# Optimization experiments

Measured on AMD Instinct MI355X. Metric: run time of the kernel, lower is better.

## Reference

```python
import jax, jax.numpy as jnp
import numpy as np

N, T, V, C, O = 64, 512, 17, 3, 64
EPS = 1e-5  # torch BatchNorm eps


def _bn(x, gamma, beta):
    # training-mode BatchNorm2d over (N, H, W) per channel, biased variance
    m = jnp.mean(x, axis=(0, 2, 3), keepdims=True)
    v = jnp.var(x, axis=(0, 2, 3), keepdims=True)
    return gamma.reshape(1, -1, 1, 1) * (x - m) * jax.lax.rsqrt(v + EPS) + beta.reshape(1, -1, 1, 1)


def setup_inputs() -> dict:
    key = jax.random.key(0)
    ks = jax.random.split(key, 20)
    f32 = jnp.float32
    PA = (jnp.eye(V, dtype=f32) / (1.0 + 1e-5))  # row-normalized identity, as in reset_parameter
    return {
        "x": jax.random.normal(ks[0], (N, T, V, C), f32),
        "w1": jax.random.normal(ks[1], (C, C), f32) * 0.5,
        "b1": jax.random.normal(ks[2], (C,), f32) * 0.1,
        "w2": jax.random.normal(ks[3], (C, C), f32) * 0.5,
        "b2": jax.random.normal(ks[4], (C,), f32) * 0.1,
        "convT_w": jax.random.normal(ks[5], (C,), f32) * 0.5,      # Conv2d(3,1,1) weight squeezed
        "convT_b": jax.random.normal(ks[6], (), f32) * 0.1,
        "convT_gamma": jnp.ones((), f32),
        "convT_beta": jnp.zeros((), f32),
        "PA": PA,
        "alpha": jnp.ones((V, V), f32),
        "conv2d_w": jax.random.normal(ks[7], (O, C), f32) * (2.0 / (O * 1 * 1)) ** 0.5,  # conv_branch_init
        "conv2d_b": jnp.zeros((O,), f32),
        "bn_gamma": jnp.full((O,), 1e-6, f32),  # bn_init(self.bn, 1e-6)
        "bn_beta": jnp.zeros((O,), f32),
        "pool_w": jax.random.normal(ks[8], (O, C), f32) * (2.0 / C) ** 0.5,  # kaiming fan_out-ish
        "pool_b": jnp.zeros((O,), f32),
        "pool_gamma": jnp.ones((O,), f32),
        "pool_beta": jnp.zeros((O,), f32),
    }


def reference(x, w1, b1, w2, b2, convT_w, convT_b, convT_gamma, convT_beta,
              PA, alpha, conv2d_w, conv2d_b, bn_gamma, bn_beta,
              pool_w, pool_b, pool_gamma, pool_beta):
    # x: (N, T, V, C)
    x1 = x @ w1.T + b1                     # linear1, (N,T,V,C)
    x2 = x @ w2.T + b2                     # linear2
    # d[n,t,i,j,c] = x1[n,t,j,c] - x2[n,t,i,c]; the 1x1 conv over C is linear,
    # so contract with convT_w BEFORE broadcasting to avoid the (N,T,V,V,C) tensor.
    a1 = x1 @ convT_w                      # (N,T,V)
    a2 = x2 @ convT_w                      # (N,T,V)
    s = a1[:, :, None, :] - a2[:, :, :, None] + convT_b   # (N,T,V,V)
    # BatchNorm2d(1): single channel -> stats over the whole tensor; then ReLU
    m = jnp.mean(s)
    var = jnp.var(s)
    s = jax.nn.relu(convT_gamma * (s - m) * jax.lax.rsqrt(var + EPS) + convT_beta)
    # temporal abs-diff, sum over T, mean over batch -> learned adjacency offset (V,V)
    a3 = jnp.mean(jnp.sum(jnp.abs(s[:, 1:] - s[:, :-1]), axis=1), axis=0)
    # NOTE: the original does x.view(N, C, T, V) -- a raw memory reinterpretation,
    # NOT a permute. Replicate with reshape.
    xr = x.reshape(N, C, T, V)
    A = PA + alpha * a3                    # (V,V)
    y = (xr.reshape(N, C * T, V) @ A).reshape(N, C, T, V)
    z = jnp.einsum('nctv,oc->notv', y, conv2d_w) + conv2d_b[None, :, None, None]
    z = _bn(z, bn_gamma, bn_beta)
    p = jnp.einsum('nctv,oc->notv', xr, pool_w) + pool_b[None, :, None, None]
    p = _bn(p, pool_gamma, pool_beta)
    out = jax.nn.relu(z + p)               # (N,O,T,V)
    return out.reshape(N, T, V, O)         # raw reshape, matching torch .reshape
```

## Files before the change

kernel.cpp:

```cpp
#include <hip/hip_runtime.h>

constexpr int Nn = 64, Tt = 512, Vv = 17, Oo = 64;
constexpr int TV  = Tt * Vv;
constexpr int CTV = 3 * TV;
constexpr int NT  = Nn * Tt;
constexpr float EPSf = 1e-5f;
constexpr int GB1 = 512;
constexpr int RPB = 64;
constexpr int NU  = 289;
constexpr int GE  = 1792;
constexpr int TCH = 256;
constexpr int K2B = 128;
constexpr int BTV = 1088;

__device__ inline int div17(int v) { return (int)(((unsigned)v * 61681u) >> 20); }

__device__ inline double wred(double v) {
#pragma unroll
  for (int o = 32; o > 0; o >>= 1) v += __shfl_down(v, o, 64);
  return v;
}

__global__ void __launch_bounds__(256) k1(
    const float* __restrict__ x,
    const float* __restrict__ w1, const float* __restrict__ b1,
    const float* __restrict__ w2, const float* __restrict__ b2,
    const float* __restrict__ cw, const float* __restrict__ cb,
    double* __restrict__ spart, float* __restrict__ gpart)
{
  __shared__ float xsA[RPB * 51];
  __shared__ float xsB[3 * BTV];
  __shared__ double dred[4][5];
  const int tid = threadIdx.x, bid = blockIdx.x;
  const int n = bid >> 3, ch = bid & 7;

  {
    const float4* src = (const float4*)(x + (size_t)bid * 3264);
    float4* dst = (float4*)xsA;
    for (int i = tid; i < 816; i += 256) dst[i] = src[i];
  }
#pragma unroll
  for (int c = 0; c < 3; ++c) {
    const float4* src = (const float4*)(x + (size_t)n * CTV + (size_t)c * TV + ch * BTV);
    float4* dst = (float4*)(xsB + c * BTV);
    for (int i = tid; i < 272; i += 256) dst[i] = src[i];
  }
  __syncthreads();

  float u1[3], u2[3];
#pragma unroll
  for (int k = 0; k < 3; ++k) {
    float s1 = 0.f, s2 = 0.f;
#pragma unroll
    for (int c = 0; c < 3; ++c) { s1 += cw[c] * w1[c * 3 + k]; s2 += cw[c] * w2[c * 3 + k]; }
    u1[k] = s1; u2[k] = s2;
  }
  float d1 = 0.f, d2 = 0.f;
#pragma unroll
  for (int c = 0; c < 3; ++c) { d1 += b1[c] * cw[c]; d2 += b2[c] * cw[c]; }
  const float bb = cb[0];

  double st[5] = {0, 0, 0, 0, 0};
  if (tid < RPB) {
    const float* rp = xsA + tid * 51;
    float A = 0.f, G = 0.f, Q1 = 0.f, Q2 = 0.f;
#pragma unroll
    for (int v = 0; v < 17; ++v) {
      float x0 = rp[v * 3], x1 = rp[v * 3 + 1], x2 = rp[v * 3 + 2];
      float va1 = fmaf(x0, u1[0], fmaf(x1, u1[1], fmaf(x2, u1[2], d1)));
      float va2 = fmaf(x0, u2[0], fmaf(x1, u2[1], fmaf(x2, u2[2], d2)));
      float g = bb - va2;
      A += va1; G += g;
      Q1 = fmaf(va1, va1, Q1); Q2 = fmaf(g, g, Q2);
    }
    st[0] = A; st[1] = G; st[2] = Q1; st[3] = Q2; st[4] = (double)A * (double)G;
  }
  {
    int wv = tid >> 6;
#pragma unroll
    for (int s = 0; s < 5; ++s) { double r = wred(st[s]); if ((tid & 63) == 0) dred[wv][s] = r; }
  }

  float* gp = gpart + (size_t)bid * GE;
#pragma unroll
  for (int pass = 0; pass < 2; ++pass) {
    int k = tid + pass * 256;
    if (k < NU) {
      int u = div17(k), up = k - u * 17;
      float h0 = 0, h1 = 0, h2 = 0, h3 = 0, h4 = 0, h5 = 0;
      for (int t = 0; t < RPB; ++t) {
        int ro = t * 17;
        float a0 = xsB[ro + u],        a1 = xsB[BTV + ro + u],  a2 = xsB[2 * BTV + ro + u];
        float b0 = xsB[ro + up],       b1 = xsB[BTV + ro + up], b2 = xsB[2 * BTV + ro + up];
        h0 = fmaf(a0, b0, h0); h1 = fmaf(a0, b1, h1); h2 = fmaf(a0, b2, h2);
        h3 = fmaf(a1, b1, h3); h4 = fmaf(a1, b2, h4); h5 = fmaf(a2, b2, h5);
      }
      gp[0 * NU + k] = h0; gp[1 * NU + k] = h1; gp[2 * NU + k] = h2;
      gp[3 * NU + k] = h3; gp[4 * NU + k] = h4; gp[5 * NU + k] = h5;
    }
  }
  if (tid < 51) {
    int c = div17(tid), u = tid - c * 17;
    float m = 0.f;
    for (int t = 0; t < RPB; ++t) m += xsB[c * BTV + t * 17 + u];
    gp[6 * NU + tid] = m;
  }
  if (tid < GE - 1785) gp[1785 + tid] = 0.f;

  __syncthreads();
  if (tid < 5)
    spart[(size_t)bid * 5 + tid] = dred[0][tid] + dred[1][tid] + dred[2][tid] + dred[3][tid];
}

__global__ void __launch_bounds__(256) k2(
    const float* __restrict__ x, const double* __restrict__ spart,
    const float* __restrict__ gpart,
    const float* __restrict__ w1, const float* __restrict__ b1,
    const float* __restrict__ w2, const float* __restrict__ b2,
    const float* __restrict__ cw, const float* __restrict__ cb,
    const float* __restrict__ cg_, const float* __restrict__ cbeta,
    float* __restrict__ a3part, double* __restrict__ gramF)
{
  __shared__ float l1[(TCH + 1) * Vv];
  __shared__ float l2[(TCH + 1) * Vv];
  __shared__ double dred[4][14];
  __shared__ float sfl[2];
  const int tid = threadIdx.x;
  const int jb = blockIdx.y * 2 + blockIdx.x;
  const int wv = tid >> 6;

  {
    double v5[5];
#pragma unroll
    for (int s = 0; s < 5; ++s)
      v5[s] = spart[(size_t)tid * 5 + s] + spart[(size_t)(tid + 256) * 5 + s];
#pragma unroll
    for (int s = 0; s < 5; ++s) { double r = wred(v5[s]); if ((tid & 63) == 0) dred[wv][s] = r; }
  }
  __syncthreads();
  if (tid == 0) {
    double S[5];
#pragma unroll
    for (int s = 0; s < 5; ++s) S[s] = dred[0][s] + dred[1][s] + dred[2][s] + dred[3][s];
    double cnt = (double)Nn * Tt * Vv * Vv;
    double mean = ((double)Vv * (S[0] + S[1])) / cnt;
    double m2   = ((double)Vv * (S[2] + S[3]) + 2.0 * S[4]) / cnt;
    double var  = m2 - mean * mean;
    double scale = (double)cg_[0] / sqrt(var + (double)EPSf);
    double shift = (double)cbeta[0] + scale * ((double)cb[0] - mean);
    sfl[0] = (float)scale; sfl[1] = (float)(shift - scale * (double)cb[0]);
  }
  __syncthreads();

  {
    int e0 = jb * 14;
    const float* g1 = gpart + (size_t)tid * GE + e0;
    const float* g2 = gpart + (size_t)(tid + 256) * GE + e0;
    double gv[14];
#pragma unroll
    for (int k = 0; k < 14; ++k) gv[k] = (double)g1[k] + (double)g2[k];
#pragma unroll
    for (int k = 0; k < 14; ++k) { double r = wred(gv[k]); if ((tid & 63) == 0) dred[wv][k] = r; }
    __syncthreads();
    if (tid < 14)
      gramF[e0 + tid] = dred[0][tid] + dred[1][tid] + dred[2][tid] + dred[3][tid];
  }

  float u1[3], u2[3];
#pragma unroll
  for (int k = 0; k < 3; ++k) {
    float s1 = 0.f, s2 = 0.f;
#pragma unroll
    for (int c = 0; c < 3; ++c) { s1 += cw[c] * w1[c * 3 + k]; s2 += cw[c] * w2[c * 3 + k]; }
    u1[k] = s1; u2[k] = s2;
  }
  float d1 = 0.f, d2 = 0.f;
#pragma unroll
  for (int c = 0; c < 3; ++c) { d1 += b1[c] * cw[c]; d2 += b2[c] * cw[c]; }
  const float bb = cb[0];

  const int n = blockIdx.y, t0 = blockIdx.x * TCH;
  int tend = t0 + TCH; if (tend > Tt - 1) tend = Tt - 1;
  const int nload = tend - t0 + 1, total = nload * 17;
  for (int idx = tid; idx < total; idx += 256) {
    int r = div17(idx), vv = idx - r * 17;
    const float* xp = x + ((size_t)((n * Tt + t0 + r) * 17 + vv)) * 3;
    float x0 = xp[0], x1 = xp[1], x2 = xp[2];
    float va1 = fmaf(x0, u1[0], fmaf(x1, u1[1], fmaf(x2, u1[2], d1)));
    float va2 = fmaf(x0, u2[0], fmaf(x1, u2[1], fmaf(x2, u2[2], d2)));
    l1[idx] = va1; l2[idx] = bb - va2;
  }
  __syncthreads();

  {
    float scale = sfl[0], c0 = sfl[1];
    for (int e = tid; e < 289; e += 256) {
      int i = div17(e), j = e - i * 17;
      float prev = fmaxf(fmaf(scale, l1[j] + l2[i], c0), 0.f), acc = 0.f;
      for (int r = 1; r < nload; ++r) {
        float cur = fmaxf(fmaf(scale, l1[r * 17 + j] + l2[r * 17 + i], c0), 0.f);
        acc += fabsf(cur - prev); prev = cur;
      }
      a3part[(size_t)jb * 289 + e] = acc;
    }
  }
}

__global__ void __launch_bounds__(256, 2) k3(
    const float* __restrict__ x,
    const float* __restrict__ PA, const float* __restrict__ alpha,
    const float* __restrict__ a3part, const double* __restrict__ gramF,
    const float* __restrict__ c2w, const float* __restrict__ c2b,
    const float* __restrict__ bng, const float* __restrict__ bnb,
    const float* __restrict__ pw, const float* __restrict__ pb,
    const float* __restrict__ pg, const float* __restrict__ pbeta,
    float* __restrict__ out)
{
  __shared__ float xs[3 * BTV], ys[3 * BTV];
  __shared__ float As[NU], Bh[NU], rsA[17], coefs[512];
  __shared__ double gs[GE], mom[18];
  const int tid = threadIdx.x, bid = blockIdx.x;
  const int n = bid >> 3, ch = bid & 7;
  const int t0c = ch * BTV;

  for (int e = tid; e < GE; e += 256) gs[e] = gramF[e];
  for (int e = tid; e < NU; e += 256) {
    float acc = 0.f;
#pragma unroll 4
    for (int j = 0; j < K2B; ++j) acc += a3part[(size_t)j * NU + e];
    As[e] = fmaf(alpha[e], acc * (1.0f / Nn), PA[e]);
  }
  __syncthreads();

  for (int k = tid; k < NU; k += 256) {
    int u = div17(k), up = k - u * 17;
    float s = 0.f;
#pragma unroll
    for (int v = 0; v < 17; ++v) s = fmaf(As[u * 17 + v], As[up * 17 + v], s);
    Bh[k] = s;
  }
  if (tid < 17) {
    float s = 0.f;
#pragma unroll
    for (int v = 0; v < 17; ++v) s += As[tid * 17 + v];
    rsA[tid] = s;
  }
  __syncthreads();

  if (tid < 6) {
    double s = 0.0;
    for (int k = 0; k < NU; ++k) s += gs[tid * NU + k] * (double)Bh[k];
    mom[3 + tid] = s;
  } else if (tid < 12) {
    int p = tid - 6; double s = 0.0;
#pragma unroll
    for (int u = 0; u < 17; ++u) s += gs[p * NU + u * 18];
    mom[12 + p] = s;
  } else if (tid < 15) {
    int c = tid - 12; double s = 0.0;
#pragma unroll
    for (int u = 0; u < 17; ++u) s += gs[6 * NU + c * 17 + u] * (double)rsA[u];
    mom[c] = s;
  } else if (tid < 18) {
    int c = tid - 15; double s = 0.0;
#pragma unroll
    for (int u = 0; u < 17; ++u) s += gs[6 * NU + c * 17 + u];
    mom[9 + c] = s;
  }
  __syncthreads();

#pragma unroll
  for (int c = 0; c < 3; ++c) {
    const float4* src = (const float4*)(x + (size_t)n * CTV + (size_t)c * TV + t0c);
    float4* dst = (float4*)(xs + c * BTV);
    for (int i = tid; i < 272; i += 256) dst[i] = src[i];
  }
  if (tid < 64) {
    int o = tid;
    const double cnt = (double)Nn * Tt * Vv;
    double my0 = mom[0] / cnt, my1 = mom[1] / cnt, my2 = mom[2] / cnt;
    double e00 = mom[3] / cnt, e01 = mom[4] / cnt, e02 = mom[5] / cnt;
    double e11 = mom[6] / cnt, e12 = mom[7] / cnt, e22 = mom[8] / cnt;
    double mx0 = mom[9] / cnt, mx1 = mom[10] / cnt, mx2 = mom[11] / cnt;
    double f00 = mom[12] / cnt, f01 = mom[13] / cnt, f02 = mom[14] / cnt;
    double f11 = mom[15] / cnt, f12 = mom[16] / cnt, f22 = mom[17] / cnt;
    double w0 = c2w[o * 3], w1_ = c2w[o * 3 + 1], w2_ = c2w[o * 3 + 2], bz = c2b[o];
    double wm = w0 * my0 + w1_ * my1 + w2_ * my2, mz = wm + bz;
    double Ez2 = w0 * w0 * e00 + 2 * w0 * w1_ * e01 + 2 * w0 * w2_ * e02
               + w1_ * w1_ * e11 + 2 * w1_ * w2_ * e12 + w2_ * w2_ * e22
               + 2 * bz * wm + bz * bz;
    double sz = (double)bng[o] / sqrt(Ez2 - mz * mz + (double)EPSf);
    double q0 = pw[o * 3], q1 = pw[o * 3 + 1], q2 = pw[o * 3 + 2], bp = pb[o];
    double qm = q0 * mx0 + q1 * mx1 + q2 * mx2, mp = qm + bp;
    double Ep2 = q0 * q0 * f00 + 2 * q0 * q1 * f01 + 2 * q0 * q2 * f02
               + q1 * q1 * f11 + 2 * q1 * q2 * f12 + q2 * q2 * f22
               + 2 * bp * qm + bp * bp;
    double sp = (double)pg[o] / sqrt(Ep2 - mp * mp + (double)EPSf);
    coefs[o * 8 + 0] = (float)(sz * w0); coefs[o * 8 + 1] = (float)(sz * w1_); coefs[o * 8 + 2] = (float)(sz * w2_);
    coefs[o * 8 + 3] = (float)(sp * q0); coefs[o * 8 + 4] = (float)(sp * q1); coefs[o * 8 + 5] = (float)(sp * q2);
    coefs[o * 8 + 6] = (float)(sz * (bz - mz) + (double)bnb[o] + sp * (bp - mp) + (double)pbeta[o]);
    coefs[o * 8 + 7] = 0.f;
  }
  __syncthreads();

#pragma unroll
  for (int k = 0; k < 5; ++k) {
    int e = k * 256 + tid;
    if (e < BTV) {
      int tr = div17(e), v = e - tr * 17;
      float y0 = 0.f, y1 = 0.f, y2 = 0.f;
#pragma unroll
      for (int u = 0; u < 17; ++u) {
        float a = As[u * 17 + v];
        y0 = fmaf(xs[tr * 17 + u], a, y0);
        y1 = fmaf(xs[BTV + tr * 17 + u], a, y1);
        y2 = fmaf(xs[2 * BTV + tr * 17 + u], a, y2);
      }
      ys[e] = y0; ys[BTV + e] = y1; ys[2 * BTV + e] = y2;
    }
  }
  __syncthreads();

  float* ob = out + (size_t)n * ((size_t)Oo * TV) + t0c;
#pragma unroll 2
  for (int k = 0; k < 68; ++k) {
    int idx = k * 256 + tid;
    int o = div17(idx >> 4);
    int q = idx - o * 272, tq = q * 4;
    float4 y0 = *(const float4*)&ys[tq];
    float4 y1 = *(const float4*)&ys[BTV + tq];
    float4 y2 = *(const float4*)&ys[2 * BTV + tq];
    float4 x0 = *(const float4*)&xs[tq];
    float4 x1 = *(const float4*)&xs[BTV + tq];
    float4 x2 = *(const float4*)&xs[2 * BTV + tq];
    float a0 = coefs[o * 8 + 0], a1 = coefs[o * 8 + 1], a2 = coefs[o * 8 + 2];
    float p0 = coefs[o * 8 + 3], p1 = coefs[o * 8 + 4], p2 = coefs[o * 8 + 5];
    float be = coefs[o * 8 + 6];
    float4 r;
    r.x = fmaxf(fmaf(a0, y0.x, fmaf(a1, y1.x, fmaf(a2, y2.x, fmaf(p0, x0.x, fmaf(p1, x1.x, fmaf(p2, x2.x, be)))))), 0.f);
    r.y = fmaxf(fmaf(a0, y0.y, fmaf(a1, y1.y, fmaf(a2, y2.y, fmaf(p0, x0.y, fmaf(p1, x1.y, fmaf(p2, x2.y, be)))))), 0.f);
    r.z = fmaxf(fmaf(a0, y0.z, fmaf(a1, y1.z, fmaf(a2, y2.z, fmaf(p0, x0.z, fmaf(p1, x1.z, fmaf(p2, x2.z, be)))))), 0.f);
    r.w = fmaxf(fmaf(a0, y0.w, fmaf(a1, y1.w, fmaf(a2, y2.w, fmaf(p0, x0.w, fmaf(p1, x1.w, fmaf(p2, x2.w, be)))))), 0.f);
    *(float4*)(ob + (size_t)o * TV + tq) = r;
  }
}

extern "C" void kernel_launch(void* const* d_in, const int* in_sizes, int n_in,
                              void* d_out, int out_size, void* d_ws, size_t ws_size,
                              hipStream_t stream)
{
  (void)in_sizes; (void)n_in; (void)out_size; (void)ws_size;
  const float* x     = (const float*)d_in[0];
  const float* w1    = (const float*)d_in[1];
  const float* b1    = (const float*)d_in[2];
  const float* w2    = (const float*)d_in[3];
  const float* b2    = (const float*)d_in[4];
  const float* cw    = (const float*)d_in[5];
  const float* cb    = (const float*)d_in[6];
  const float* cg_   = (const float*)d_in[7];
  const float* cbeta = (const float*)d_in[8];
  const float* PA    = (const float*)d_in[9];
  const float* alpha = (const float*)d_in[10];
  const float* c2w   = (const float*)d_in[11];
  const float* c2b   = (const float*)d_in[12];
  const float* bng   = (const float*)d_in[13];
  const float* bnb   = (const float*)d_in[14];
  const float* pw    = (const float*)d_in[15];
  const float* pb    = (const float*)d_in[16];
  const float* pg    = (const float*)d_in[17];
  const float* pbeta = (const float*)d_in[18];
  float* out = (float*)d_out;

  char* ws = (char*)d_ws;
  double* spart  = (double*)(ws + 0);
  float*  gpart  = (float*)(ws + 20480);
  float*  a3part = (float*)(ws + 3690496);
  double* gramF  = (double*)(ws + 3838464);

  hipLaunchKernelGGL(k1, dim3(GB1), dim3(256), 0, stream,
                     x, w1, b1, w2, b2, cw, cb, spart, gpart);
  hipLaunchKernelGGL(k2, dim3(2, Nn), dim3(256), 0, stream,
                     x, spart, gpart, w1, b1, w2, b2, cw, cb, cg_, cbeta, a3part, gramF);
  hipLaunchKernelGGL(k3, dim3(512), dim3(256), 0, stream,
                     x, PA, alpha, a3part, gramF, c2w, c2b, bng, bnb,
                     pw, pb, pg, pbeta, out);
}
```

Measured before the change: 87.64 us.

## Restructure k2 to one block per batch with segmented temporal sums

k2 now uses one block per batch element instead of two T-chunks. It loads the whole sequence into shared memory and splits each of the 289 adjacency entries' temporal abs-diff scan into 8 segments spread across threads, which raises parallelism over the old one-entry-per-thread serial loop. a3part is transposed to an entry-major layout, so k3 reduces 64 partials per entry with float4 loads instead of 128 strided loads. k3 also starts the x tile load before the adjacency setup, parallelizes the Gram-times-Bh moment dot product across 32 lanes with shuffles, and drops one barrier. The cost is fewer k2 blocks (64) with larger shared-memory use, which may reduce occupancy.

```diff
diff --git a/kernel.cpp b/kernel.cpp
--- a/kernel.cpp
+++ b/kernel.cpp
@@ -3,14 +3,11 @@
 constexpr int Nn = 64, Tt = 512, Vv = 17, Oo = 64;
 constexpr int TV  = Tt * Vv;
 constexpr int CTV = 3 * TV;
-constexpr int NT  = Nn * Tt;
 constexpr float EPSf = 1e-5f;
 constexpr int GB1 = 512;
 constexpr int RPB = 64;
 constexpr int NU  = 289;
 constexpr int GE  = 1792;
-constexpr int TCH = 256;
-constexpr int K2B = 128;
 constexpr int BTV = 1088;
 
 __device__ inline int div17(int v) { return (int)(((unsigned)v * 61681u) >> 20); }
@@ -121,12 +118,13 @@
     const float* __restrict__ cg_, const float* __restrict__ cbeta,
     float* __restrict__ a3part, double* __restrict__ gramF)
 {
-  __shared__ float l1[(TCH + 1) * Vv];
-  __shared__ float l2[(TCH + 1) * Vv];
-  __shared__ double dred[4][14];
+  __shared__ float l1[Tt * Vv];
+  __shared__ float l2[Tt * Vv];
+  __shared__ float segsum[NU * 8];
+  __shared__ double dred[4][28];
   __shared__ float sfl[2];
   const int tid = threadIdx.x;
-  const int jb = blockIdx.y * 2 + blockIdx.x;
+  const int n = blockIdx.x;
   const int wv = tid >> 6;
 
   {
@@ -153,16 +151,16 @@
   __syncthreads();
 
   {
-    int e0 = jb * 14;
+    int e0 = n * 28;
     const float* g1 = gpart + (size_t)tid * GE + e0;
     const float* g2 = gpart + (size_t)(tid + 256) * GE + e0;
-    double gv[14];
-#pragma unroll
-    for (int k = 0; k < 14; ++k) gv[k] = (double)g1[k] + (double)g2[k];
-#pragma unroll
-    for (int k = 0; k < 14; ++k) { double r = wred(gv[k]); if ((tid & 63) == 0) dred[wv][k] = r; }
+    double gv[28];
+#pragma unroll
+    for (int k = 0; k < 28; ++k) gv[k] = (double)g1[k] + (double)g2[k];
+#pragma unroll
+    for (int k = 0; k < 28; ++k) { double r = wred(gv[k]); if ((tid & 63) == 0) dred[wv][k] = r; }
     __syncthreads();
-    if (tid < 14)
+    if (tid < 28)
       gramF[e0 + tid] = dred[0][tid] + dred[1][tid] + dred[2][tid] + dred[3][tid];
   }
 
@@ -179,12 +177,9 @@
   for (int c = 0; c < 3; ++c) { d1 += b1[c] * cw[c]; d2 += b2[c] * cw[c]; }
   const float bb = cb[0];
 
-  const int n = blockIdx.y, t0 = blockIdx.x * TCH;
-  int tend = t0 + TCH; if (tend > Tt - 1) tend = Tt - 1;
-  const int nload = tend - t0 + 1, total = nload * 17;
-  for (int idx = tid; idx < total; idx += 256) {
-    int r = div17(idx), vv = idx - r * 17;
-    const float* xp = x + ((size_t)((n * Tt + t0 + r) * 17 + vv)) * 3;
+  const float* xb = x + (size_t)n * CTV;
+  for (int idx = tid; idx < Tt * Vv; idx += 256) {
+    const float* xp = xb + idx * 3;
     float x0 = xp[0], x1 = xp[1], x2 = xp[2];
     float va1 = fmaf(x0, u1[0], fmaf(x1, u1[1], fmaf(x2, u1[2], d1)));
     float va2 = fmaf(x0, u2[0], fmaf(x1, u2[1], fmaf(x2, u2[2], d2)));
@@ -193,16 +188,28 @@
   __syncthreads();
 
   {
-    float scale = sfl[0], c0 = sfl[1];
-    for (int e = tid; e < 289; e += 256) {
+    const float scale = sfl[0], c0 = sfl[1];
+    for (int task = tid; task < NU * 8; task += 256) {
+      int e = task >> 3, s = task & 7;
       int i = div17(e), j = e - i * 17;
-      float prev = fmaxf(fmaf(scale, l1[j] + l2[i], c0), 0.f), acc = 0.f;
-      for (int r = 1; r < nload; ++r) {
-        float cur = fmaxf(fmaf(scale, l1[r * 17 + j] + l2[r * 17 + i], c0), 0.f);
+      int r0 = s * 64;
+      int dmax = (s == 7) ? (Tt - 1) : (r0 + 64);
+      float prev = fmaxf(fmaf(scale, l1[r0 * 17 + j] + l2[r0 * 17 + i], c0), 0.f);
+      float acc = 0.f;
+      for (int d = r0 + 1; d <= dmax; ++d) {
+        float cur = fmaxf(fmaf(scale, l1[d * 17 + j] + l2[d * 17 + i], c0), 0.f);
         acc += fabsf(cur - prev); prev = cur;
       }
-      a3part[(size_t)jb * 289 + e] = acc;
+      segsum[e * 8 + s] = acc;
     }
+  }
+  __syncthreads();
+
+  for (int e = tid; e < NU; e += 256) {
+    float s = 0.f;
+#pragma unroll
+    for (int k = 0; k < 8; ++k) s += segsum[e * 8 + k];
+    a3part[(size_t)e * Nn + n] = s;
   }
 }
 
@@ -218,56 +225,11 @@
 {
   __shared__ float xs[3 * BTV], ys[3 * BTV];
   __shared__ float As[NU], Bh[NU], rsA[17], coefs[512];
-  __shared__ double gs[GE], mom[18];
+  __shared__ double gs[GE];
+  __shared__ double mom[18];
   const int tid = threadIdx.x, bid = blockIdx.x;
   const int n = bid >> 3, ch = bid & 7;
   const int t0c = ch * BTV;
-
-  for (int e = tid; e < GE; e += 256) gs[e] = gramF[e];
-  for (int e = tid; e < NU; e += 256) {
-    float acc = 0.f;
-#pragma unroll 4
-    for (int j = 0; j < K2B; ++j) acc += a3part[(size_t)j * NU + e];
-    As[e] = fmaf(alpha[e], acc * (1.0f / Nn), PA[e]);
-  }
-  __syncthreads();
-
-  for (int k = tid; k < NU; k += 256) {
-    int u = div17(k), up = k - u * 17;
-    float s = 0.f;
-#pragma unroll
-    for (int v = 0; v < 17; ++v) s = fmaf(As[u * 17 + v], As[up * 17 + v], s);
-    Bh[k] = s;
-  }
-  if (tid < 17) {
-    float s = 0.f;
-#pragma unroll
-    for (int v = 0; v < 17; ++v) s += As[tid * 17 + v];
-    rsA[tid] = s;
-  }
-  __syncthreads();
-
-  if (tid < 6) {
-    double s = 0.0;
-    for (int k = 0; k < NU; ++k) s += gs[tid * NU + k] * (double)Bh[k];
-    mom[3 + tid] = s;
-  } else if (tid < 12) {
-    int p = tid - 6; double s = 0.0;
-#pragma unroll
-    for (int u = 0; u < 17; ++u) s += gs[p * NU + u * 18];
-    mom[12 + p] = s;
-  } else if (tid < 15) {
-    int c = tid - 12; double s = 0.0;
-#pragma unroll
-    for (int u = 0; u < 17; ++u) s += gs[6 * NU + c * 17 + u] * (double)rsA[u];
-    mom[c] = s;
-  } else if (tid < 18) {
-    int c = tid - 15; double s = 0.0;
-#pragma unroll
-    for (int u = 0; u < 17; ++u) s += gs[6 * NU + c * 17 + u];
-    mom[9 + c] = s;
-  }
-  __syncthreads();
 
 #pragma unroll
   for (int c = 0; c < 3; ++c) {
@@ -275,6 +237,61 @@
     float4* dst = (float4*)(xs + c * BTV);
     for (int i = tid; i < 272; i += 256) dst[i] = src[i];
   }
+
+  for (int e = tid; e < GE; e += 256) gs[e] = gramF[e];
+  for (int e = tid; e < NU; e += 256) {
+    const float4* ap = (const float4*)(a3part + (size_t)e * Nn);
+    float4 a4 = ap[0];
+#pragma unroll
+    for (int q = 1; q < 16; ++q) {
+      float4 b4 = ap[q];
+      a4.x += b4.x; a4.y += b4.y; a4.z += b4.z; a4.w += b4.w;
+    }
+    float acc = (a4.x + a4.y) + (a4.z + a4.w);
+    As[e] = fmaf(alpha[e], acc * (1.0f / Nn), PA[e]);
+  }
+  __syncthreads();
+
+  for (int k = tid; k < NU; k += 256) {
+    int u = div17(k), up = k - u * 17;
+    float s = 0.f;
+#pragma unroll
+    for (int v = 0; v < 17; ++v) s = fmaf(As[u * 17 + v], As[up * 17 + v], s);
+    Bh[k] = s;
+  }
+  if (tid < 17) {
+    float s = 0.f;
+#pragma unroll
+    for (int v = 0; v < 17; ++v) s += As[tid * 17 + v];
+    rsA[tid] = s;
+  }
+  __syncthreads();
+
+  if (tid < 192) {
+    int p = tid >> 5, r = tid & 31;
+    double s = 0.0;
+    for (int k = r; k < NU; k += 32) s += gs[p * NU + k] * (double)Bh[k];
+#pragma unroll
+    for (int off = 16; off > 0; off >>= 1) s += __shfl_down(s, off, 32);
+    if (r == 0) mom[3 + p] = s;
+  } else if (tid < 198) {
+    int p = tid - 192; double s = 0.0;
+#pragma unroll
+    for (int u = 0; u < 17; ++u) s += gs[p * NU + u * 18];
+    mom[12 + p] = s;
+  } else if (tid < 201) {
+    int c = tid - 198; double s = 0.0;
+#pragma unroll
+    for (int u = 0; u < 17; ++u) s += gs[6 * NU + c * 17 + u] * (double)rsA[u];
+    mom[c] = s;
+  } else if (tid < 204) {
+    int c = tid - 201; double s = 0.0;
+#pragma unroll
+    for (int u = 0; u < 17; ++u) s += gs[6 * NU + c * 17 + u];
+    mom[9 + c] = s;
+  }
+  __syncthreads();
+
   if (tid < 64) {
     int o = tid;
     const double cnt = (double)Nn * Tt * Vv;
@@ -301,8 +318,6 @@
     coefs[o * 8 + 6] = (float)(sz * (bz - mz) + (double)bnb[o] + sp * (bp - mp) + (double)pbeta[o]);
     coefs[o * 8 + 7] = 0.f;
   }
-  __syncthreads();
-
 #pragma unroll
   for (int k = 0; k < 5; ++k) {
     int e = k * 256 + tid;
@@ -375,11 +390,11 @@
   double* spart  = (double*)(ws + 0);
   float*  gpart  = (float*)(ws + 20480);
   float*  a3part = (float*)(ws + 3690496);
-  double* gramF  = (double*)(ws + 3838464);
+  double* gramF  = (double*)(ws + 3764480);
 
   hipLaunchKernelGGL(k1, dim3(GB1), dim3(256), 0, stream,
                      x, w1, b1, w2, b2, cw, cb, spart, gpart);
-  hipLaunchKernelGGL(k2, dim3(2, Nn), dim3(256), 0, stream,
+  hipLaunchKernelGGL(k2, dim3(Nn), dim3(256), 0, stream,
                      x, spart, gpart, w1, b1, w2, b2, cw, cb, cg_, cbeta, a3part, gramF);
   hipLaunchKernelGGL(k3, dim3(512), dim3(256), 0, stream,
                      x, PA, alpha, a3part, gramF, c2w, c2b, bng, bnb,
```

After: 111.8 us. +27.5%, slower.
